# Kernel optimization log

Measured on AMD Instinct MI355X. Metric: run time of the kernel, lower is better.

The kernel has to match this reference:

```python
import jax, jax.numpy as jnp
from jax import lax
import numpy as np

B, L, D, H, SH = 4, 1024, 512, 8, 256
MLP_H = 4 * D
GAMMA, BETA = 0.1, 1.0
SIG_A, SIG_B = 1.0, 0.5
BIG = 1e9


def setup_inputs() -> dict:
    key = jax.random.key(0)
    ks = jax.random.split(key, 8)

    def lin(k, fin, fout):
        return jax.random.normal(k, (fin, fout), jnp.float32) * (1.0 / np.sqrt(fin))

    inp = {}
    inp["x"] = jax.random.normal(ks[0], (B, L, D), jnp.float32)
    inp["ln1_g"] = jnp.ones((D,), jnp.float32)
    inp["ln1_b"] = jnp.zeros((D,), jnp.float32)
    inp["ln2_g"] = jnp.ones((D,), jnp.float32)
    inp["ln2_b"] = jnp.zeros((D,), jnp.float32)
    inp["qkv_w"] = lin(ks[1], D, 3 * D)
    inp["qkv_b"] = jnp.zeros((3 * D,), jnp.float32)
    inp["proj_w"] = lin(ks[2], D, D)
    inp["proj_b"] = jnp.zeros((D,), jnp.float32)
    inp["fc1_w"] = lin(ks[3], D, MLP_H)
    inp["fc1_b"] = jnp.zeros((MLP_H,), jnp.float32)
    inp["fc2_w"] = lin(ks[4], MLP_H, D)
    inp["fc2_b"] = jnp.zeros((D,), jnp.float32)
    # 4 SigmaNets (norm1, attn, norm2, mlp) stacked on leading axis
    inp["sig_w1"] = jax.random.normal(ks[5], (4, D, SH), jnp.float32) * (1.0 / np.sqrt(D))
    inp["sig_b1"] = jnp.zeros((4, SH), jnp.float32)
    inp["sig_w2"] = jax.random.normal(ks[6], (4, SH, D), jnp.float32) * (1.0 / np.sqrt(SH))
    inp["sig_b2"] = jnp.zeros((4, D), jnp.float32)
    return inp


def layernorm(x, g, b, eps=1e-5):
    m = x.mean(-1, keepdims=True)
    v = ((x - m) ** 2).mean(-1, keepdims=True)
    return (x - m) / jnp.sqrt(v + eps) * g + b


def sigmanet(x, w1, b1, w2, b2):
    # (B,L,D) -> (B,L,1), sigma = a*sigmoid(mean(fc2(relu(fc1(x))))) + b
    h = jax.nn.relu(x @ w1 + b1)
    o = h @ w2 + b2
    m = o.mean(-1, keepdims=True)
    return SIG_A * jax.nn.sigmoid(m) + SIG_B


def attention(x, qkv_w, qkv_b, proj_w, proj_b):
    b_, l_, d_ = x.shape
    hd = d_ // H
    qkv = (x @ qkv_w + qkv_b).reshape(b_, l_, 3, H, hd)
    q, k, v = qkv[:, :, 0], qkv[:, :, 1], qkv[:, :, 2]  # (B,L,H,hd)
    scores = jnp.einsum("bqhd,bkhd->bhqk", q, k) * (hd ** -0.5)
    attn = jax.nn.softmax(scores, axis=-1)
    out = jnp.einsum("bhqk,bkhd->bqhd", attn, v).reshape(b_, l_, d_)
    return out @ proj_w + proj_b


def mlp(x, fc1_w, fc1_b, fc2_w, fc2_b):
    return jax.nn.gelu(x @ fc1_w + fc1_b, approximate=False) @ fc2_w + fc2_b


def soft_dtw(C, gamma):
    # soft-min DP over (B, N, N) cost matrix via anti-diagonal scan
    b_, n_, m_ = C.shape
    i_arr = jnp.arange(n_)

    def step(carry, k):
        d2, d1 = carry  # diagonals k-2, k-1; entry i holds R[i, (k-?)-i]
        j = k - i_arr
        valid = (j >= 0) & (j < m_)
        jc = jnp.clip(j, 0, m_ - 1)
        Cd = jnp.where(valid[None, :], C[:, i_arr, jc], BIG)
        pad = jnp.full((b_, 1), BIG, C.dtype)
        a = jnp.concatenate([pad, d2[:, :-1]], axis=1)  # R[i-1, j-1]
        a = a.at[:, 0].set(jnp.where(k == 0, 0.0, a[:, 0]))  # virtual R[-1,-1]=0
        bdiag = jnp.concatenate([pad, d1[:, :-1]], axis=1)  # R[i-1, j]
        c = d1  # R[i, j-1]
        smin = -gamma * jax.nn.logsumexp(-jnp.stack([a, bdiag, c], 0) / gamma, axis=0)
        new = jnp.where(valid[None, :], Cd + smin, BIG)
        return (d1, new), None

    init = (jnp.full((b_, n_), BIG, C.dtype), jnp.full((b_, n_), BIG, C.dtype))
    (_, last), _ = lax.scan(step, init, jnp.arange(n_ + m_ - 1))
    return last[:, n_ - 1]  # R[N-1, M-1]


def udtw(x, y, sx, sy):
    # pairwise squared distances without (B,L,L,D) intermediate
    x2 = jnp.sum(x * x, -1)  # (B,L)
    y2 = jnp.sum(y * y, -1)
    Dm = x2[:, :, None] + y2[:, None, :] - 2.0 * jnp.einsum("bnd,bmd->bnm", x, y)
    Dm = jnp.maximum(Dm, 0.0)
    Sig = sx ** 2 + jnp.swapaxes(sy, 1, 2) ** 2  # (B,L,L) sigma_i^2 + sigma_j^2
    d = soft_dtw(Dm / Sig, GAMMA)               # uncertainty-weighted distance path
    s = soft_dtw(BETA * jnp.log(Sig), GAMMA)    # sigma regularization path
    return d, s


def reference(x, ln1_g, ln1_b, ln2_g, ln2_b, qkv_w, qkv_b, proj_w, proj_b,
              fc1_w, fc1_b, fc2_w, fc2_b, sig_w1, sig_b1, sig_w2, sig_b2):
    orig = x
    attn_out = attention(layernorm(x, ln1_g, ln1_b), qkv_w, qkv_b, proj_w, proj_b)
    sigma_x = sigmanet(orig, sig_w1[0], sig_b1[0], sig_w2[0], sig_b2[0])
    sigma_attn = sigmanet(attn_out, sig_w1[1], sig_b1[1], sig_w2[1], sig_b2[1])
    d_a, s_a = udtw(orig, attn_out, sigma_x, sigma_attn)
    x = x + attn_out * sigma_attn  # merge_mode == 'mul'
    mlp_out = mlp(layernorm(x, ln2_g, ln2_b), fc1_w, fc1_b, fc2_w, fc2_b)
    sigma_x2 = sigmanet(orig, sig_w1[2], sig_b1[2], sig_w2[2], sig_b2[2])
    sigma_mlp = sigmanet(mlp_out, sig_w1[3], sig_b1[3], sig_w2[3], sig_b2[3])
    d_m, s_m = udtw(orig, mlp_out, sigma_x2, sigma_mlp)
    l_ = x.shape[1]
    aux_loss = (d_a.mean() + s_a.mean() + d_m.mean() + s_m.mean()) / (l_ * l_)
    x = x + mlp_out * sigma_mlp
    return x, aux_loss
```

## Files before the change

### kernel.cpp

```cpp
#include <hip/hip_runtime.h>
#include <math.h>

typedef unsigned short ushort;
typedef __attribute__((ext_vector_type(8))) short short8;
typedef __attribute__((ext_vector_type(4))) short short4v;
typedef __attribute__((ext_vector_type(4))) float f32x4;

#define DEVI static __device__ __forceinline__

constexpr int Bq = 4, Lq = 1024, Dq = 512, Hq = 8, SHq = 256;
constexpr int Mrows = Bq * Lq;
constexpr float BIGF = 1e9f;
constexpr int PSTR = 1048576 + 16;

DEVI float bf2f(ushort u) { union { unsigned u; float f; } v; v.u = ((unsigned)u) << 16; return v.f; }
DEVI float bf2f(short s) { return bf2f((ushort)s); }
DEVI ushort f2bf(float f) {
  union { float f; unsigned u; } v; v.f = f;
  unsigned r = v.u + 0x7fffu + ((v.u >> 16) & 1u);
  return (ushort)(r >> 16);
}
DEVI float wave_sum(float x) { for (int o = 1; o < 64; o <<= 1) x += __shfl_xor(x, o, 64); return x; }
DEVI float readin(const void* p, long i, int isf32) {
  return isf32 ? ((const float*)p)[i] : bf2f(((const ushort*)p)[i]);
}
DEVI float sigm05(float x) { return 1.f / (1.f + __expf(-x)) + 0.5f; }

DEVI void gload16(const ushort* g, ushort* l) {
  __builtin_amdgcn_global_load_lds((const __attribute__((address_space(1))) unsigned*)g,
                                   (__attribute__((address_space(3))) unsigned*)l, 16, 0, 0);
}

__global__ void detect_kern(const unsigned* __restrict__ g, int* __restrict__ flag) {
  if (threadIdx.x == 0) flag[0] = (g[0] == 0x3F800000u) ? 1 : 0;
}

struct PrepArgs {
  const void *ln1_g, *ln1_b, *ln2_g, *ln2_b, *qkv_b, *proj_b, *fc1_b, *fc2_b, *sig_b1;
  ushort* csmall;
  const void* x_raw; ushort* x_bf;
  const void *qkv_w, *proj_w, *fc1_w, *fc2_w, *sig_w1;
  ushort *wt_qkv, *wt_proj, *wt_fc1, *wt_fc2, *wt_sig1;
  const void *sig_w2;
  const void *sig_b2;
  float *w2bar, *b2bar;
  float *zbuf;
  const int* flag;
};

DEVI void do_transpose(const void* src, ushort* dst, int R, int C, int bx, int by, int bz, int f,
                       ushort (*t)[65]) {
  const int tx = threadIdx.x & 63, tg = threadIdx.x >> 6;
  const long base = (long)bz * R * C;
  const int r0 = by * 64, c0 = bx * 64;
#pragma unroll
  for (int i = 0; i < 16; ++i) {
    int y = tg * 16 + i;
    float v = readin(src, base + (long)(r0 + y) * C + c0 + tx, f);
    t[y][tx] = f2bf(v);
  }
  __syncthreads();
#pragma unroll
  for (int i = 0; i < 16; ++i) {
    int y = tg * 16 + i;
    dst[base + (long)(c0 + y) * R + r0 + tx] = t[tx][y];
  }
}

__global__ __launch_bounds__(256) void prep_kern(PrepArgs a) {
  __shared__ ushort t[64][65];
  const int bid = blockIdx.x, tid = threadIdx.x;
  const int f = *a.flag;
  if (bid < 9) {
    const int off[10] = {0, 512, 1024, 1536, 2048, 3584, 4096, 6144, 6656, 7680};
    const void* ps[9] = {a.ln1_g, a.ln1_b, a.ln2_g, a.ln2_b, a.qkv_b, a.proj_b, a.fc1_b, a.fc2_b, a.sig_b1};
    const void* s = ps[bid];
    const int n = off[bid + 1] - off[bid];
    for (int i = tid; i < n; i += 256)
      a.csmall[off[bid] + i] = f ? f2bf(((const float*)s)[i]) : ((const ushort*)s)[i];
  } else if (bid < 2057) {
    const long c0 = (long)(bid - 9) * 1024;
    for (int i = tid; i < 1024; i += 256)
      a.x_bf[c0 + i] = f ? f2bf(((const float*)a.x_raw)[c0 + i]) : ((const ushort*)a.x_raw)[c0 + i];
  } else if (bid < 2313) {
    const int wid = tid >> 6, lane = tid & 63;
    const int p = (bid - 2057) * 4 + wid;
    const int k = p & 255, s = p >> 8;
    float acc = 0.f;
#pragma unroll
    for (int i = 0; i < 8; ++i) acc += readin(a.sig_w2, ((long)s * SHq + k) * Dq + lane * 8 + i, f);
    acc = wave_sum(acc);
    if (lane == 0) a.w2bar[s * SHq + k] = acc * (1.f / Dq);
  } else if (bid < 2314) {
    const int wid = tid >> 6, lane = tid & 63;
    float acc = 0.f;
#pragma unroll
    for (int i = 0; i < 8; ++i) acc += readin(a.sig_b2, (long)wid * Dq + lane * 8 + i, f);
    acc = wave_sum(acc);
    if (lane == 0) a.b2bar[wid] = acc * (1.f / Dq);
  } else if (bid < 2506) {
    const int lb = bid - 2314;
    do_transpose(a.qkv_w, a.wt_qkv, 512, 1536, lb % 24, lb / 24, 0, f, t);
  } else if (bid < 2570) {
    const int lb = bid - 2506;
    do_transpose(a.proj_w, a.wt_proj, 512, 512, lb % 8, lb / 8, 0, f, t);
  } else if (bid < 2826) {
    const int lb = bid - 2570;
    do_transpose(a.fc1_w, a.wt_fc1, 512, 2048, lb % 32, lb / 32, 0, f, t);
  } else if (bid < 3082) {
    const int lb = bid - 2826;
    do_transpose(a.fc2_w, a.wt_fc2, 2048, 512, lb % 8, lb / 8, 0, f, t);
  } else if (bid < 3210) {
    const int lb = bid - 3082;
    const int z = lb / 32, rem = lb % 32;
    do_transpose(a.sig_w1, a.wt_sig1, 512, 256, rem % 4, rem / 4, z, f, t);
  } else {
    const int base = (bid - 3210) * 1024;
    for (int i = tid; i < 1024; i += 256) a.zbuf[base + i] = 0.f;
  }
}

__global__ __launch_bounds__(256) void ln_kern(const ushort* __restrict__ x, const ushort* __restrict__ g,
                                               const ushort* __restrict__ b, ushort* __restrict__ out,
                                               float* __restrict__ x2out) {
  const int row = blockIdx.x * 4 + (threadIdx.x >> 6);
  const int lane = threadIdx.x & 63;
  short8 v = *(const short8*)(x + (long)row * Dq + lane * 8);
  float f[8]; float s = 0.f, s2 = 0.f;
#pragma unroll
  for (int i = 0; i < 8; ++i) { f[i] = bf2f(v[i]); s += f[i]; s2 += f[i] * f[i]; }
  s = wave_sum(s); s2 = wave_sum(s2);
  if (lane == 0) x2out[row] = s2;
  float mean = s * (1.f / Dq);
  float var = s2 * (1.f / Dq) - mean * mean;
  float rstd = rsqrtf(var + 1e-5f);
  short8 gv = *(const short8*)(g + lane * 8);
  short8 bv = *(const short8*)(b + lane * 8);
  short8 o;
#pragma unroll
  for (int i = 0; i < 8; ++i) o[i] = (short)f2bf((f[i] - mean) * rstd * bf2f(gv[i]) + bf2f(bv[i]));
  *(short8*)(out + (long)row * Dq + lane * 8) = o;
}

template<int EPI>
__global__ __launch_bounds__(256) void gemm_kern(
    const ushort* __restrict__ A, int lda, long sA,
    const ushort* __restrict__ Bt, int ldb, long sB,
    const ushort* __restrict__ bias,
    void* __restrict__ Cout, int ldc, long sC, int K,
    float* __restrict__ ysq,
    const float* __restrict__ w2bar_base, float* __restrict__ sdot, int setBase, int setStep,
    const float* __restrict__ vx2, const float* __restrict__ vy2,
    const float* __restrict__ dotx, const float* __restrict__ doty,
    const float* __restrict__ b2bar, int setx, int sety) {
  __shared__ alignas(16) ushort As[128 * 32];
  __shared__ alignas(16) ushort Bs[128 * 32];
  const int tid = threadIdx.x, lane = tid & 63, wid = tid >> 6;
  const int wr = wid >> 1, wc = wid & 1;
  const int m0 = blockIdx.y * 128, n0 = blockIdx.x * 128;
  const int bz = blockIdx.z;
  const ushort* Ab = A + (long)bz * sA;
  const ushort* Bb = Bt + (long)bz * sB;
  const int lr = lane & 15, lk = (lane >> 4) * 8;
  const int srow = lane >> 2, scol = (lane & 3) * 8;
  f32x4 acc[4][4];
#pragma unroll
  for (int i = 0; i < 4; ++i)
#pragma unroll
    for (int j = 0; j < 4; ++j) acc[i][j] = f32x4{0.f, 0.f, 0.f, 0.f};

  for (int k0 = 0; k0 < K; k0 += 32) {
    __syncthreads();
    {
      const int rA0 = wid * 16, rA1 = wid * 16 + 64;
      gload16(Ab + (long)(m0 + rA0 + srow) * lda + k0 + scol, &As[rA0 * 32]);
      gload16(Ab + (long)(m0 + rA1 + srow) * lda + k0 + scol, &As[rA1 * 32]);
      gload16(Bb + (long)(n0 + rA0 + srow) * ldb + k0 + scol, &Bs[rA0 * 32]);
      gload16(Bb + (long)(n0 + rA1 + srow) * ldb + k0 + scol, &Bs[rA1 * 32]);
    }
    __syncthreads();
    short8 af[4], bg[4];
#pragma unroll
    for (int m = 0; m < 4; ++m) af[m] = *(const short8*)&As[(wr * 64 + m * 16 + lr) * 32 + lk];
#pragma unroll
    for (int n = 0; n < 4; ++n) bg[n] = *(const short8*)&Bs[(wc * 64 + n * 16 + lr) * 32 + lk];
#pragma unroll
    for (int m = 0; m < 4; ++m)
#pragma unroll
      for (int n = 0; n < 4; ++n)
        acc[m][n] = __builtin_amdgcn_mfma_f32_16x16x32_bf16(af[m], bg[n], acc[m][n], 0, 0, 0);
  }
  const int lq = (lane >> 4) * 4;
  const int set = (EPI == 1) ? (setBase + bz * setStep) : 0;
  float pd[4][4];
  if (EPI == 1 || (EPI == 0 && ysq != nullptr)) {
#pragma unroll
    for (int m = 0; m < 4; ++m)
#pragma unroll
      for (int q = 0; q < 4; ++q) pd[m][q] = 0.f;
  }
#pragma unroll
  for (int n = 0; n < 4; ++n) {
    const int col = n0 + wc * 64 + n * 16 + lr;
    float bia = 0.f, y2v = 0.f, syv = 0.f, w2v = 0.f;
    if (EPI == 0 || EPI == 2) { if (bias) bia = bf2f(bias[col]); }
    if (EPI == 1) { bia = bf2f(bias[set * 256 + col]); w2v = w2bar_base[set * SHq + col]; }
    if (EPI == 3) {
      y2v = vy2[(long)bz * Lq + col];
      float t = sigm05(doty[(long)bz * Lq + col] + b2bar[sety]);
      syv = t * t;
    }
#pragma unroll
    for (int m = 0; m < 4; ++m) {
      f32x4 v = acc[m][n];
      if (EPI == 0 || EPI == 2) {
#pragma unroll
        for (int q = 0; q < 4; ++q) {
          const int row = m0 + wr * 64 + m * 16 + lq + q;
          float c = v[q] + bia;
          if (EPI == 2) c = 0.5f * c * (1.f + erff(c * 0.70710678118654752f));
          ushort cb = f2bf(c);
          ((ushort*)Cout)[(long)bz * sC + (long)row * ldc + col] = cb;
          if (EPI == 0 && ysq != nullptr) { float cr = bf2f(cb); pd[m][q] += cr * cr; }
        }
      } else if (EPI == 1) {
#pragma unroll
        for (int q = 0; q < 4; ++q) {
          float c = fmaxf(v[q] + bia, 0.f);
          pd[m][q] += f2bf(c) == 0 ? 0.f : bf2f(f2bf(c)) * w2v;
        }
      } else {
        const int row0 = m0 + wr * 64 + m * 16 + lq;
        f32x4 o;
#pragma unroll
        for (int q = 0; q < 4; ++q) {
          float x2v = vx2[(long)bz * Lq + row0 + q];
          float t = sigm05(dotx[(long)bz * Lq + row0 + q] + b2bar[setx]);
          float dm = fmaxf(x2v + y2v - 2.f * v[q], 0.f);
          o[q] = dm / (t * t + syv);
        }
        *(f32x4*)((float*)Cout + (long)bz * sC + (long)col * 1024 + row0) = o;
      }
    }
  }
  if (EPI == 1 || (EPI == 0 && ysq != nullptr)) {
#pragma unroll
    for (int m = 0; m < 4; ++m)
#pragma unroll
      for (int q = 0; q < 4; ++q) {
#pragma unroll
        for (int o = 1; o < 16; o <<= 1) pd[m][q] += __shfl_xor(pd[m][q], o, 64);
        if (lr == 0) {
          const int row = m0 + wr * 64 + m * 16 + lq + q;
          if (EPI == 1) atomicAdd(&sdot[(long)set * Mrows + row], pd[m][q]);
          else          atomicAdd(&ysq[row], pd[m][q]);
        }
      }
  }
}

__global__ __launch_bounds__(256) void attn_kern(const ushort* __restrict__ qkv, ushort* __restrict__ octx) {
  const int qt = blockIdx.x, h = blockIdx.y, b = blockIdx.z;
  const int tid = threadIdx.x, lane = tid & 63, wid = tid >> 6;
  const int lr = lane & 15, lkg = lane >> 4;
  __shared__ alignas(16) short Ks[64 * 72];
  __shared__ alignas(16) short Vt[64 * 72];
  __shared__ alignas(16) short Ps[64 * 72];
  const long qrow0 = (long)b * Lq + qt * 64;
  short8 qf[2];
  {
    const ushort* qp = qkv + (qrow0 + wid * 16 + lr) * 1536 + h * 64;
    qf[0] = *(const short8*)(qp + lkg * 8);
    qf[1] = *(const short8*)(qp + 32 + lkg * 8);
  }
  f32x4 accO[4];
#pragma unroll
  for (int n = 0; n < 4; ++n) accO[n] = f32x4{0.f, 0.f, 0.f, 0.f};
  float mrun[4], lrun[4];
#pragma unroll
  for (int q = 0; q < 4; ++q) { mrun[q] = -1e30f; lrun[q] = 0.f; }

  for (int t = 0; t < 16; ++t) {
    __syncthreads();
#pragma unroll
    for (int i = 0; i < 2; ++i) {
      const int row = (tid >> 3) + i * 32;
      const int c8 = (tid & 7) * 8;
      const long gr = ((long)b * Lq + t * 64 + row) * 1536 + h * 64;
      short8 kv = *(const short8*)(qkv + gr + 512 + c8);
      *(short8*)&Ks[row * 72 + c8] = kv;
      short8 vv = *(const short8*)(qkv + gr + 1024 + c8);
#pragma unroll
      for (int j = 0; j < 8; ++j) Vt[(c8 + j) * 72 + row] = vv[j];
    }
    __syncthreads();
    f32x4 sf[4];
#pragma unroll
    for (int n = 0; n < 4; ++n) {
      sf[n] = f32x4{0.f, 0.f, 0.f, 0.f};
#pragma unroll
      for (int ks = 0; ks < 2; ++ks) {
        short8 bk = *(const short8*)&Ks[(n * 16 + lr) * 72 + ks * 32 + lkg * 8];
        sf[n] = __builtin_amdgcn_mfma_f32_16x16x32_bf16(qf[ks], bk, sf[n], 0, 0, 0);
      }
    }
#pragma unroll
    for (int n = 0; n < 4; ++n)
#pragma unroll
      for (int q = 0; q < 4; ++q) sf[n][q] *= 0.125f;
    float scl[4];
#pragma unroll
    for (int q = 0; q < 4; ++q) {
      float mx = fmaxf(fmaxf(sf[0][q], sf[1][q]), fmaxf(sf[2][q], sf[3][q]));
#pragma unroll
      for (int o = 1; o < 16; o <<= 1) mx = fmaxf(mx, __shfl_xor(mx, o, 64));
      float mnew = fmaxf(mrun[q], mx);
      scl[q] = __expf(mrun[q] - mnew);
      mrun[q] = mnew;
      float rs = 0.f;
#pragma unroll
      for (int n = 0; n < 4; ++n) { float pp = __expf(sf[n][q] - mnew); sf[n][q] = pp; rs += pp; }
#pragma unroll
      for (int o = 1; o < 16; o <<= 1) rs += __shfl_xor(rs, o, 64);
      lrun[q] = lrun[q] * scl[q] + rs;
    }
#pragma unroll
    for (int n = 0; n < 4; ++n)
#pragma unroll
      for (int q = 0; q < 4; ++q) accO[n][q] *= scl[q];
#pragma unroll
    for (int n = 0; n < 4; ++n)
#pragma unroll
      for (int q = 0; q < 4; ++q)
        Ps[(wid * 16 + lkg * 4 + q) * 72 + n * 16 + lr] = (short)f2bf(sf[n][q]);
    short8 pa[2];
    pa[0] = *(const short8*)&Ps[(wid * 16 + lr) * 72 + lkg * 8];
    pa[1] = *(const short8*)&Ps[(wid * 16 + lr) * 72 + 32 + lkg * 8];
#pragma unroll
    for (int n = 0; n < 4; ++n)
#pragma unroll
      for (int ks = 0; ks < 2; ++ks) {
        short8 bv = *(const short8*)&Vt[(n * 16 + lr) * 72 + ks * 32 + lkg * 8];
        accO[n] = __builtin_amdgcn_mfma_f32_16x16x32_bf16(pa[ks], bv, accO[n], 0, 0, 0);
      }
  }
#pragma unroll
  for (int n = 0; n < 4; ++n) {
    const int col = h * 64 + n * 16 + lr;
#pragma unroll
    for (int q = 0; q < 4; ++q) {
      const long row = qrow0 + wid * 16 + lkg * 4 + q;
      octx[row * 512 + col] = f2bf(accO[n][q] / fmaxf(lrun[q], 1e-30f));
    }
  }
}

__global__ __launch_bounds__(256) void fuse1_kern(const ushort* __restrict__ x, const ushort* __restrict__ attn,
                                                  const float* __restrict__ sdot1, const float* __restrict__ b2bar,
                                                  const ushort* __restrict__ g,
                                                  const ushort* __restrict__ bb, void* __restrict__ x1out,
                                                  ushort* __restrict__ xn2, const int* __restrict__ flag) {
  const int row = blockIdx.x * 4 + (threadIdx.x >> 6), lane = threadIdx.x & 63;
  const int isf32 = *flag;
  const float sg = sigm05(sdot1[row] + b2bar[1]);
  short8 xv = *(const short8*)(x + (long)row * Dq + lane * 8);
  short8 av = *(const short8*)(attn + (long)row * Dq + lane * 8);
  float f[8]; float s = 0.f, s2 = 0.f;
#pragma unroll
  for (int i = 0; i < 8; ++i) {
    f[i] = bf2f(xv[i]) + bf2f(av[i]) * sg;
    s += f[i]; s2 += f[i] * f[i];
  }
  if (isf32) {
    float* o32 = (float*)x1out + (long)row * Dq + lane * 8;
    *(f32x4*)o32 = f32x4{f[0], f[1], f[2], f[3]};
    *(f32x4*)(o32 + 4) = f32x4{f[4], f[5], f[6], f[7]};
  } else {
    short8 xo;
#pragma unroll
    for (int i = 0; i < 8; ++i) xo[i] = (short)f2bf(f[i]);
    *(short8*)((ushort*)x1out + (long)row * Dq + lane * 8) = xo;
  }
  s = wave_sum(s); s2 = wave_sum(s2);
  float mean = s * (1.f / Dq);
  float var = s2 * (1.f / Dq) - mean * mean;
  float rstd = rsqrtf(var + 1e-5f);
  short8 gv = *(const short8*)(g + lane * 8);
  short8 bv = *(const short8*)(bb + lane * 8);
  short8 o;
#pragma unroll
  for (int i = 0; i < 8; ++i) o[i] = (short)f2bf((f[i] - mean) * rstd * bf2f(gv[i]) + bf2f(bv[i]));
  *(short8*)(xn2 + (long)row * Dq + lane * 8) = o;
}

__global__ __launch_bounds__(256) void fuse2_kern(const ushort* __restrict__ mlp,
                                                  const float* __restrict__ sdot3, const float* __restrict__ b2bar,
                                                  void* __restrict__ out, const int* __restrict__ flag) {
  const int row = blockIdx.x * 4 + (threadIdx.x >> 6), lane = threadIdx.x & 63;
  const int isf32 = *flag;
  const float sg = sigm05(sdot3[row] + b2bar[3]);
  short8 mv = *(const short8*)(mlp + (long)row * Dq + lane * 8);
  if (isf32) {
    float* o32 = (float*)out + (long)row * Dq + lane * 8;
    f32x4 a = *(const f32x4*)o32;
    f32x4 b = *(const f32x4*)(o32 + 4);
#pragma unroll
    for (int i = 0; i < 4; ++i) a[i] += bf2f(mv[i]) * sg;
#pragma unroll
    for (int i = 0; i < 4; ++i) b[i] += bf2f(mv[4 + i]) * sg;
    *(f32x4*)o32 = a;
    *(f32x4*)(o32 + 4) = b;
  } else {
    ushort* o16 = (ushort*)out + (long)row * Dq + lane * 8;
    short8 xv = *(const short8*)o16;
    short8 o;
#pragma unroll
    for (int i = 0; i < 8; ++i) o[i] = (short)f2bf(bf2f(xv[i]) + bf2f(mv[i]) * sg);
    *(short8*)o16 = o;
  }
}

__global__ __launch_bounds__(128, 1) void dtw_kern(const float* __restrict__ Cta, const float* __restrict__ Ctm,
                                                   const float* __restrict__ sdot, const float* __restrict__ b2bar,
                                                   float* __restrict__ res) {
  const int sid = blockIdx.x >> 2, b = blockIdx.x & 3;
  const int tid = threadIdx.x, lane = tid & 63, wid = tid >> 6;
  const bool isS = (sid & 1);
  __shared__ alignas(16) float smemf[18432];
  constexpr float LN2 = 0.69314718055994531f;

  float cur[16];
#pragma unroll
  for (int r = 0; r < 16; ++r) cur[r] = BIGF;
  float A = BIGF;
  float B = BIGF;
  float D = (lane == 0) ? 0.f : BIGF;

  if (!isS) {
    const float* Ct = ((sid == 0) ? Cta : Ctm) + (long)b * PSTR;

#define PRODUCE2(S0)                                                           \
    {                                                                          \
      f32x4 L[4][8];                                                           \
      _Pragma("unroll")                                                        \
      for (int j = 0; j < 4; ++j) {                                            \
        const int ss = (S0) + j;                                               \
        int cA = 2 * ss - 2 * lane;                                            \
        int cB = cA + 1;                                                       \
        cA = cA < 0 ? 0 : (cA > 1023 ? 1023 : cA);                             \
        cB = cB < 0 ? 0 : (cB > 1023 ? 1023 : cB);                             \
        const float* gA = Ct + (long)cA * 1024 + lane * 16;                    \
        const float* gB = Ct + (long)cB * 1024 + lane * 16;                    \
        _Pragma("unroll")                                                      \
        for (int q = 0; q < 4; ++q) { L[j][q] = *(const f32x4*)(gA + q * 4);   \
                                      L[j][4 + q] = *(const f32x4*)(gB + q * 4); } \
      }                                                                        \
      __builtin_amdgcn_sched_barrier(0);                                       \
      _Pragma("unroll")                                                        \
      for (int j = 0; j < 4; ++j) {                                            \
        float* lp = &smemf[(((S0) + j) & 7) * 2304 + lane * 36];               \
        _Pragma("unroll")                                                      \
        for (int q = 0; q < 4; ++q) { *(f32x4*)(lp + q * 4) = L[j][q];         \
                                      *(f32x4*)(lp + 16 + q * 4) = L[j][4 + q]; } \
      }                                                                        \
    }

#define LOADR(RA, RB, S)                                                       \
    {                                                                          \
      const float* lp = &smemf[((S) & 7) * 2304 + lane * 36];                  \
      _Pragma("unroll")                                                        \
      for (int q = 0; q < 4; ++q) { RA[q] = *(const f32x4*)(lp + q * 4);       \
                                    RB[q] = *(const f32x4*)(lp + 16 + q * 4); } \
    }

#define DCHAIN2(S, RA, RB, CHK)                                                \
    {                                                                          \
      const int c1 = 2 * (S) - 2 * lane;                                       \
      const bool v1 = (unsigned)c1 < 1024u;                                    \
      const bool v2 = (unsigned)(c1 + 1) < 1024u;                              \
      float above = A, diag = D;                                               \
      _Pragma("unroll")                                                        \
      for (int i = 0; i < 16; ++i) {                                           \
        float tmp = cur[i];                                                    \
        float v = RA[i >> 2][i & 3] + fminf(fminf(above, tmp), diag);          \
        cur[i] = (CHK) ? (v1 ? v : tmp) : v;                                   \
        diag = tmp; above = v;                                                 \
      }                                                                        \
      float bot1 = cur[15];                                                    \
      above = B; diag = A;                                                     \
      _Pragma("unroll")                                                        \
      for (int i = 0; i < 16; ++i) {                                           \
        float tmp = cur[i];                                                    \
        float v = RB[i >> 2][i & 3] + fminf(fminf(above, tmp), diag);          \
        cur[i] = (CHK) ? (v2 ? v : tmp) : v;                                   \
        diag = tmp; above = v;                                                 \
      }                                                                        \
      float bot2 = cur[15];                                                    \
      D = B;                                                                   \
      float sA = __shfl_up(bot1, 1, 64);                                       \
      float sB = __shfl_up(bot2, 1, 64);                                       \
      A = (lane == 0) ? BIGF : sA;                                             \
      B = (lane == 0) ? BIGF : sB;                                             \
    }

#define DPHASE4(S0, CHK)                                                       \
    {                                                                          \
      f32x4 pa[4], pb[4], qa[4], qb[4];                                        \
      LOADR(pa, pb, (S0) + 0)                                                  \
      LOADR(qa, qb, (S0) + 1)                                                  \
      DCHAIN2((S0) + 0, pa, pb, CHK)                                           \
      LOADR(pa, pb, (S0) + 2)                                                  \
      DCHAIN2((S0) + 1, qa, qb, CHK)                                           \
      LOADR(qa, qb, (S0) + 3)                                                  \
      DCHAIN2((S0) + 2, pa, pb, CHK)                                           \
      DCHAIN2((S0) + 3, qa, qb, CHK)                                           \
    }

    if (wid == 1) PRODUCE2(0)
    __syncthreads();
#pragma clang loop unroll(disable)
    for (int p = 0; p < 16; ++p) {
      if (wid == 1) { PRODUCE2(4 * p + 4) } else { DPHASE4(4 * p, 1) }
      __syncthreads();
    }
#pragma clang loop unroll(disable)
    for (int p = 16; p < 128; ++p) {
      if (wid == 1) { PRODUCE2(4 * p + 4) } else { DPHASE4(4 * p, 0) }
      __syncthreads();
    }
#pragma clang loop unroll(disable)
    for (int p = 128; p < 144; ++p) {
      if (wid == 1) { if (p < 143) PRODUCE2(4 * p + 4) } else { DPHASE4(4 * p, 1) }
      __syncthreads();
    }
#undef PRODUCE2
#undef LOADR
#undef DCHAIN2
#undef DPHASE4
    if (wid == 0 && lane == 63) res[blockIdx.x] = cur[15];
  } else {
    const int sxset = (sid == 1) ? 0 : 2;
    const float bx2 = b2bar[sxset], by2 = b2bar[sxset + 1];
    const float* dx = sdot + (long)sxset * Mrows + b * Lq;
    const float* dy = sdot + (long)(sxset + 1) * Mrows + b * Lq;
    for (int i = tid; i < Lq; i += 128) { float v = sigm05(dy[i] + by2); smemf[i] = v * v; }
    __syncthreads();
    if (wid == 1) return;
    float sx2[16];
#pragma unroll
    for (int r = 0; r < 16; ++r) { float t = sigm05(dx[16 * lane + r] + bx2); sx2[r] = t * t; }
    int ia = -2 * lane; ia = ia < 0 ? 0 : ia;
    int ib = 1 - 2 * lane; ib = ib < 0 ? 0 : ib;
    float syA = smemf[ia], syB = smemf[ib];

#define SSTEP2(S, CHK)                                                         \
    {                                                                          \
      int na = 2 * ((S) + 1) - 2 * lane; na = na < 0 ? 0 : (na > 1023 ? 1023 : na); \
      int nb = na + 1; nb = nb > 1023 ? 1023 : nb;                             \
      float syA_n = smemf[na], syB_n = smemf[nb];                              \
      const int c1 = 2 * (S) - 2 * lane;                                       \
      const bool v1 = (unsigned)c1 < 1024u;                                    \
      const bool v2 = (unsigned)(c1 + 1) < 1024u;                              \
      float above = A, diag = D;                                               \
      _Pragma("unroll")                                                        \
      for (int i = 0; i < 16; ++i) {                                           \
        float tmp = cur[i];                                                    \
        float cv = LN2 * __builtin_amdgcn_logf(sx2[i] + syA);                  \
        float v = cv + fminf(fminf(above, tmp), diag);                         \
        cur[i] = (CHK) ? (v1 ? v : tmp) : v;                                   \
        diag = tmp; above = v;                                                 \
      }                                                                        \
      float bot1 = cur[15];                                                    \
      above = B; diag = A;                                                     \
      _Pragma("unroll")                                                        \
      for (int i = 0; i < 16; ++i) {                                           \
        float tmp = cur[i];                                                    \
        float cv = LN2 * __builtin_amdgcn_logf(sx2[i] + syB);                  \
        float v = cv + fminf(fminf(above, tmp), diag);                         \
        cur[i] = (CHK) ? (v2 ? v : tmp) : v;                                   \
        diag = tmp; above = v;                                                 \
      }                                                                        \
      float bot2 = cur[15];                                                    \
      D = B; syA = syA_n; syB = syB_n;                                         \
      float sA = __shfl_up(bot1, 1, 64);                                       \
      float sB = __shfl_up(bot2, 1, 64);                                       \
      A = (lane == 0) ? BIGF : sA;                                             \
      B = (lane == 0) ? BIGF : sB;                                             \
    }

#pragma clang loop unroll(disable)
    for (int s = 0; s < 63; ++s) SSTEP2(s, 1)
#pragma clang loop unroll(disable)
    for (int s = 63; s < 512; ++s) SSTEP2(s, 0)
#pragma clang loop unroll(disable)
    for (int s = 512; s < 576; ++s) SSTEP2(s, 1)
#undef SSTEP2
    if (lane == 63) res[blockIdx.x] = cur[15];
  }
}

__global__ void aux_kern(const float* __restrict__ res, void* __restrict__ out,
                         const int* __restrict__ flag) {
  if (threadIdx.x == 0) {
    float s = 0.f;
    for (int i = 0; i < 16; ++i) s += res[i];
    float v = s * (0.25f / (1024.f * 1024.f));
    if (*flag) ((float*)out)[(size_t)Mrows * 512] = v;
    else       ((ushort*)out)[(size_t)Mrows * 512] = f2bf(v);
  }
}

extern "C" void kernel_launch(void* const* d_in, const int* in_sizes, int n_in,
                              void* d_out, int out_size, void* d_ws, size_t ws_size,
                              hipStream_t stream) {
  const void* x_raw   = d_in[0];
  const void* ln1_g   = d_in[1];
  const void* ln1_b   = d_in[2];
  const void* ln2_g   = d_in[3];
  const void* ln2_b   = d_in[4];
  const void* qkv_w   = d_in[5];
  const void* qkv_b   = d_in[6];
  const void* proj_w  = d_in[7];
  const void* proj_b  = d_in[8];
  const void* fc1_w   = d_in[9];
  const void* fc1_b   = d_in[10];
  const void* fc2_w   = d_in[11];
  const void* fc2_b   = d_in[12];
  const void* sig_w1  = d_in[13];
  const void* sig_b1  = d_in[14];
  const void* sig_w2  = d_in[15];
  const void* sig_b2  = d_in[16];

  char* p = (char*)d_ws;
  auto alloc = [&](size_t n) { char* r = p; p += (n + 255) & ~(size_t)255; return r; };
  const size_t REGION = (size_t)4 * PSTR * 4;
  int*    flag    = (int*)alloc(256);
  ushort* csmall  = (ushort*)alloc(7680 * 2);
  ushort* x_bf    = (ushort*)alloc((size_t)Mrows * 512 * 2);
  ushort* wt_qkv  = (ushort*)alloc((size_t)1536 * 512 * 2);
  ushort* wt_proj = (ushort*)alloc((size_t)512 * 512 * 2);
  ushort* wt_fc1  = (ushort*)alloc((size_t)2048 * 512 * 2);
  ushort* wt_fc2  = (ushort*)alloc((size_t)512 * 2048 * 2);
  ushort* wt_sig1 = (ushort*)alloc((size_t)4 * 256 * 512 * 2);
  float*  w2bar   = (float*)alloc(4 * 256 * 4);
  float*  b2bar   = (float*)alloc(4 * 4);
  ushort* xnorm   = (ushort*)alloc((size_t)Mrows * 512 * 2);
  char* region1 = alloc(REGION);
  ushort* qkvb     = (ushort*)region1;
  ushort* attn_ctx = (ushort*)(region1 + (size_t)Mrows * 1536 * 2);
  float*  Cta      = (float*)region1;
  ushort* abuf   = (ushort*)alloc((size_t)Mrows * 512 * 2);
  float*  sdot   = (float*)alloc((size_t)4 * Mrows * 4);
  float*  y2a    = (float*)alloc(Mrows * 4);
  float*  y2m    = (float*)alloc(Mrows * 4);
  float*  x2n    = (float*)alloc(Mrows * 4);
  char* region2 = alloc(REGION);
  ushort* h1  = (ushort*)region2;
  float*  Ctm = (float*)region2;
  float*  dres = (float*)alloc(64 * 4);

  const ushort* c_ln1g = csmall + 0;
  const ushort* c_ln1b = csmall + 512;
  const ushort* c_ln2g = csmall + 1024;
  const ushort* c_ln2b = csmall + 1536;
  const ushort* c_qkvb = csmall + 2048;
  const ushort* c_projb = csmall + 3584;
  const ushort* c_fc1b = csmall + 4096;
  const ushort* c_fc2b = csmall + 6144;
  const ushort* c_sigb1 = csmall + 6656;

  detect_kern<<<1, 64, 0, stream>>>((const unsigned*)ln1_g, flag);
  PrepArgs pa;
  pa.ln1_g = ln1_g; pa.ln1_b = ln1_b; pa.ln2_g = ln2_g; pa.ln2_b = ln2_b;
  pa.qkv_b = qkv_b; pa.proj_b = proj_b; pa.fc1_b = fc1_b; pa.fc2_b = fc2_b; pa.sig_b1 = sig_b1;
  pa.csmall = csmall; pa.x_raw = x_raw; pa.x_bf = x_bf;
  pa.qkv_w = qkv_w; pa.proj_w = proj_w; pa.fc1_w = fc1_w; pa.fc2_w = fc2_w; pa.sig_w1 = sig_w1;
  pa.wt_qkv = wt_qkv; pa.wt_proj = wt_proj; pa.wt_fc1 = wt_fc1; pa.wt_fc2 = wt_fc2; pa.wt_sig1 = wt_sig1;
  pa.sig_w2 = sig_w2; pa.sig_b2 = sig_b2; pa.w2bar = w2bar; pa.b2bar = b2bar;
  pa.zbuf = sdot; pa.flag = flag;
  prep_kern<<<3234, 256, 0, stream>>>(pa);

  ln_kern<<<Mrows / 4, 256, 0, stream>>>(x_bf, c_ln1g, c_ln1b, xnorm, x2n);
  gemm_kern<0><<<dim3(12, 32, 1), 256, 0, stream>>>(xnorm, 512, 0, wt_qkv, 512, 0, c_qkvb,
      qkvb, 1536, 0, 512, nullptr, nullptr, nullptr, 0, 0, nullptr, nullptr, nullptr, nullptr, nullptr, 0, 0);
  attn_kern<<<dim3(16, 8, 4), 256, 0, stream>>>(qkvb, attn_ctx);
  gemm_kern<0><<<dim3(4, 32, 1), 256, 0, stream>>>(attn_ctx, 512, 0, wt_proj, 512, 0, c_projb,
      abuf, 512, 0, 512, y2a, nullptr, nullptr, 0, 0, nullptr, nullptr, nullptr, nullptr, nullptr, 0, 0);
  gemm_kern<1><<<dim3(2, 32, 2), 256, 0, stream>>>(x_bf, 512, 0, wt_sig1, 512, (long)2 * 256 * 512, c_sigb1,
      nullptr, 0, 0, 512, nullptr, w2bar, sdot, 0, 2, nullptr, nullptr, nullptr, nullptr, nullptr, 0, 0);
  gemm_kern<1><<<dim3(2, 32, 1), 256, 0, stream>>>(abuf, 512, 0, wt_sig1 + 1 * 256 * 512, 512, 0, c_sigb1,
      nullptr, 0, 0, 512, nullptr, w2bar, sdot, 1, 0, nullptr, nullptr, nullptr, nullptr, nullptr, 0, 0);
  gemm_kern<3><<<dim3(8, 8, 4), 256, 0, stream>>>(x_bf, 512, (long)1024 * 512, abuf, 512, (long)1024 * 512, nullptr,
      Cta, 1024, (long)PSTR, 512, nullptr, nullptr, nullptr, 0, 0, x2n, y2a, sdot, sdot + Mrows, b2bar, 0, 1);
  fuse1_kern<<<Mrows / 4, 256, 0, stream>>>(x_bf, abuf, sdot + Mrows, b2bar, c_ln2g, c_ln2b, d_out, xnorm, flag);
  gemm_kern<2><<<dim3(16, 32, 1), 256, 0, stream>>>(xnorm, 512, 0, wt_fc1, 512, 0, c_fc1b,
      h1, 2048, 0, 512, nullptr, nullptr, nullptr, 0, 0, nullptr, nullptr, nullptr, nullptr, nullptr, 0, 0);
  gemm_kern<0><<<dim3(4, 32, 1), 256, 0, stream>>>(h1, 2048, 0, wt_fc2, 2048, 0, c_fc2b,
      abuf, 512, 0, 2048, y2m, nullptr, nullptr, 0, 0, nullptr, nullptr, nullptr, nullptr, nullptr, 0, 0);
  gemm_kern<1><<<dim3(2, 32, 1), 256, 0, stream>>>(abuf, 512, 0, wt_sig1 + 3 * 256 * 512, 512, 0, c_sigb1,
      nullptr, 0, 0, 512, nullptr, w2bar, sdot, 3, 0, nullptr, nullptr, nullptr, nullptr, nullptr, 0, 0);
  gemm_kern<3><<<dim3(8, 8, 4), 256, 0, stream>>>(x_bf, 512, (long)1024 * 512, abuf, 512, (long)1024 * 512, nullptr,
      Ctm, 1024, (long)PSTR, 512, nullptr, nullptr, nullptr, 0, 0, x2n, y2m, sdot + 2 * Mrows, sdot + 3 * Mrows, b2bar, 2, 3);
  fuse2_kern<<<Mrows / 4, 256, 0, stream>>>(abuf, sdot + 3 * Mrows, b2bar, d_out, flag);
  dtw_kern<<<16, 128, 0, stream>>>(Cta, Ctm, sdot, b2bar, dres);
  aux_kern<<<1, 64, 0, stream>>>(dres, d_out, flag);
}
```

Before: 497.5 us.

## Process four DTW columns per wavefront step and fold aux reduction into DTW kernel

The DTW wavefront now advances four columns per lane per step instead of two. That halves the number of lane-shift steps and block barriers in the serial chain (319 steps instead of 576 half-steps). The producer warp stages four column slices into a 4-deep LDS ring, and LDS use shrinks slightly. The separate aux_kern launch is removed: the last finishing DTW block, detected with an atomic counter reset in detect_kern, sums the 16 results and writes the aux loss. The wider diagonal skew adds more wasted masked work at the start and end, and holds more registers per step.

```diff
diff --git a/kernel.cpp b/kernel.cpp
--- a/kernel.cpp
+++ b/kernel.cpp
@@ -31,8 +31,12 @@
                                    (__attribute__((address_space(3))) unsigned*)l, 16, 0, 0);
 }
 
-__global__ void detect_kern(const unsigned* __restrict__ g, int* __restrict__ flag) {
-  if (threadIdx.x == 0) flag[0] = (g[0] == 0x3F800000u) ? 1 : 0;
+__global__ void detect_kern(const unsigned* __restrict__ g, int* __restrict__ flag,
+                            float* res, unsigned* cnt) {
+  const int t = threadIdx.x;
+  if (t == 0) flag[0] = (g[0] == 0x3F800000u) ? 1 : 0;
+  if (t < 16) res[t] = 0.f;
+  if (t == 16) *cnt = 0u;
 }
 
 struct PrepArgs {
@@ -422,122 +426,100 @@
 
 __global__ __launch_bounds__(128, 1) void dtw_kern(const float* __restrict__ Cta, const float* __restrict__ Ctm,
                                                    const float* __restrict__ sdot, const float* __restrict__ b2bar,
-                                                   float* __restrict__ res) {
+                                                   float* res, unsigned* cnt,
+                                                   void* __restrict__ out, const int* __restrict__ flag) {
   const int sid = blockIdx.x >> 2, b = blockIdx.x & 3;
   const int tid = threadIdx.x, lane = tid & 63, wid = tid >> 6;
   const bool isS = (sid & 1);
-  __shared__ alignas(16) float smemf[18432];
+  __shared__ alignas(16) float smemf[17408];
   constexpr float LN2 = 0.69314718055994531f;
+  constexpr int NSTEP = 319;
 
   float cur[16];
 #pragma unroll
   for (int r = 0; r < 16; ++r) cur[r] = BIGF;
-  float A = BIGF;
-  float B = BIGF;
+  float A0 = BIGF, A1 = BIGF, A2 = BIGF, A3 = BIGF;
   float D = (lane == 0) ? 0.f : BIGF;
 
   if (!isS) {
     const float* Ct = ((sid == 0) ? Cta : Ctm) + (long)b * PSTR;
 
-#define PRODUCE2(S0)                                                           \
+#define PRODUCE4(S)                                                            \
     {                                                                          \
-      f32x4 L[4][8];                                                           \
+      f32x4 L[16];                                                             \
       _Pragma("unroll")                                                        \
       for (int j = 0; j < 4; ++j) {                                            \
-        const int ss = (S0) + j;                                               \
-        int cA = 2 * ss - 2 * lane;                                            \
-        int cB = cA + 1;                                                       \
-        cA = cA < 0 ? 0 : (cA > 1023 ? 1023 : cA);                             \
-        cB = cB < 0 ? 0 : (cB > 1023 ? 1023 : cB);                             \
-        const float* gA = Ct + (long)cA * 1024 + lane * 16;                    \
-        const float* gB = Ct + (long)cB * 1024 + lane * 16;                    \
+        int c = 4 * (S) + j - 4 * lane;                                        \
+        c = c < 0 ? 0 : (c > 1023 ? 1023 : c);                                 \
+        const float* gp = Ct + (long)c * 1024 + lane * 16;                     \
         _Pragma("unroll")                                                      \
-        for (int q = 0; q < 4; ++q) { L[j][q] = *(const f32x4*)(gA + q * 4);   \
-                                      L[j][4 + q] = *(const f32x4*)(gB + q * 4); } \
+        for (int q = 0; q < 4; ++q) L[j * 4 + q] = *(const f32x4*)(gp + q * 4);\
       }                                                                        \
       __builtin_amdgcn_sched_barrier(0);                                       \
+      float* lp = &smemf[((S) & 3) * 4352 + lane * 68];                        \
       _Pragma("unroll")                                                        \
-      for (int j = 0; j < 4; ++j) {                                            \
-        float* lp = &smemf[(((S0) + j) & 7) * 2304 + lane * 36];               \
+      for (int j = 0; j < 4; ++j)                                              \
         _Pragma("unroll")                                                      \
-        for (int q = 0; q < 4; ++q) { *(f32x4*)(lp + q * 4) = L[j][q];         \
-                                      *(f32x4*)(lp + 16 + q * 4) = L[j][4 + q]; } \
-      }                                                                        \
-    }
-
-#define LOADR(RA, RB, S)                                                       \
+        for (int q = 0; q < 4; ++q) *(f32x4*)(lp + j * 16 + q * 4) = L[j * 4 + q]; \
+    }
+
+#define DCOL(RV, AV, DV, VC, CHK)                                              \
     {                                                                          \
-      const float* lp = &smemf[((S) & 7) * 2304 + lane * 36];                  \
-      _Pragma("unroll")                                                        \
-      for (int q = 0; q < 4; ++q) { RA[q] = *(const f32x4*)(lp + q * 4);       \
-                                    RB[q] = *(const f32x4*)(lp + 16 + q * 4); } \
-    }
-
-#define DCHAIN2(S, RA, RB, CHK)                                                \
-    {                                                                          \
-      const int c1 = 2 * (S) - 2 * lane;                                       \
-      const bool v1 = (unsigned)c1 < 1024u;                                    \
-      const bool v2 = (unsigned)(c1 + 1) < 1024u;                              \
-      float above = A, diag = D;                                               \
+      float above = AV, diag = DV;                                             \
       _Pragma("unroll")                                                        \
       for (int i = 0; i < 16; ++i) {                                           \
         float tmp = cur[i];                                                    \
-        float v = RA[i >> 2][i & 3] + fminf(fminf(above, tmp), diag);          \
-        cur[i] = (CHK) ? (v1 ? v : tmp) : v;                                   \
+        float v = RV[i >> 2][i & 3] + fminf(fminf(above, tmp), diag);          \
+        cur[i] = (CHK) ? ((VC) ? v : tmp) : v;                                 \
         diag = tmp; above = v;                                                 \
       }                                                                        \
-      float bot1 = cur[15];                                                    \
-      above = B; diag = A;                                                     \
+    }
+
+#define DSTEP4(S, CHK)                                                         \
+    {                                                                          \
+      const float* lp = &smemf[((S) & 3) * 4352 + lane * 68];                  \
+      f32x4 R0[4], R1[4], R2[4], R3[4];                                        \
       _Pragma("unroll")                                                        \
-      for (int i = 0; i < 16; ++i) {                                           \
-        float tmp = cur[i];                                                    \
-        float v = RB[i >> 2][i & 3] + fminf(fminf(above, tmp), diag);          \
-        cur[i] = (CHK) ? (v2 ? v : tmp) : v;                                   \
-        diag = tmp; above = v;                                                 \
-      }                                                                        \
-      float bot2 = cur[15];                                                    \
-      D = B;                                                                   \
-      float sA = __shfl_up(bot1, 1, 64);                                       \
-      float sB = __shfl_up(bot2, 1, 64);                                       \
-      A = (lane == 0) ? BIGF : sA;                                             \
-      B = (lane == 0) ? BIGF : sB;                                             \
-    }
-
-#define DPHASE4(S0, CHK)                                                       \
-    {                                                                          \
-      f32x4 pa[4], pb[4], qa[4], qb[4];                                        \
-      LOADR(pa, pb, (S0) + 0)                                                  \
-      LOADR(qa, qb, (S0) + 1)                                                  \
-      DCHAIN2((S0) + 0, pa, pb, CHK)                                           \
-      LOADR(pa, pb, (S0) + 2)                                                  \
-      DCHAIN2((S0) + 1, qa, qb, CHK)                                           \
-      LOADR(qa, qb, (S0) + 3)                                                  \
-      DCHAIN2((S0) + 2, pa, pb, CHK)                                           \
-      DCHAIN2((S0) + 3, qa, qb, CHK)                                           \
-    }
-
-    if (wid == 1) PRODUCE2(0)
+      for (int q = 0; q < 4; ++q) { R0[q] = *(const f32x4*)(lp + q * 4);       \
+                                    R1[q] = *(const f32x4*)(lp + 16 + q * 4);  \
+                                    R2[q] = *(const f32x4*)(lp + 32 + q * 4);  \
+                                    R3[q] = *(const f32x4*)(lp + 48 + q * 4); }\
+      const int c0 = 4 * (S) - 4 * lane;                                       \
+      const bool v0 = (unsigned)c0 < 1024u;                                    \
+      const bool v1 = (unsigned)(c0 + 1) < 1024u;                              \
+      const bool v2 = (unsigned)(c0 + 2) < 1024u;                              \
+      const bool v3 = (unsigned)(c0 + 3) < 1024u;                              \
+      DCOL(R0, A0, D, v0, CHK)  float b0 = cur[15];                            \
+      DCOL(R1, A1, A0, v1, CHK) float b1 = cur[15];                            \
+      DCOL(R2, A2, A1, v2, CHK) float b2 = cur[15];                            \
+      DCOL(R3, A3, A2, v3, CHK) float b3 = cur[15];                            \
+      D = A3;                                                                  \
+      float s0 = __shfl_up(b0, 1, 64), s1 = __shfl_up(b1, 1, 64);              \
+      float s2 = __shfl_up(b2, 1, 64), s3 = __shfl_up(b3, 1, 64);              \
+      A0 = (lane == 0) ? BIGF : s0; A1 = (lane == 0) ? BIGF : s1;              \
+      A2 = (lane == 0) ? BIGF : s2; A3 = (lane == 0) ? BIGF : s3;              \
+    }
+
+    if (wid == 1) { PRODUCE4(0) PRODUCE4(1) PRODUCE4(2) }
     __syncthreads();
 #pragma clang loop unroll(disable)
-    for (int p = 0; p < 16; ++p) {
-      if (wid == 1) { PRODUCE2(4 * p + 4) } else { DPHASE4(4 * p, 1) }
+    for (int p = 0; p < 63; ++p) {
+      if (wid == 1) { PRODUCE4(p + 3) } else { DSTEP4(p, 1) }
       __syncthreads();
     }
 #pragma clang loop unroll(disable)
-    for (int p = 16; p < 128; ++p) {
-      if (wid == 1) { PRODUCE2(4 * p + 4) } else { DPHASE4(4 * p, 0) }
+    for (int p = 63; p < 256; ++p) {
+      if (wid == 1) { PRODUCE4(p + 3) } else { DSTEP4(p, 0) }
       __syncthreads();
     }
 #pragma clang loop unroll(disable)
-    for (int p = 128; p < 144; ++p) {
-      if (wid == 1) { if (p < 143) PRODUCE2(4 * p + 4) } else { DPHASE4(4 * p, 1) }
+    for (int p = 256; p < NSTEP; ++p) {
+      if (wid == 1) { if (p + 3 < NSTEP) PRODUCE4(p + 3) } else { DSTEP4(p, 1) }
       __syncthreads();
     }
-#undef PRODUCE2
-#undef LOADR
-#undef DCHAIN2
-#undef DPHASE4
-    if (wid == 0 && lane == 63) res[blockIdx.x] = cur[15];
+#undef PRODUCE4
+#undef DCOL
+#undef DSTEP4
   } else {
     const int sxset = (sid == 1) ? 0 : 2;
     const float bx2 = b2bar[sxset], by2 = b2bar[sxset + 1];
@@ -545,68 +527,67 @@
     const float* dy = sdot + (long)(sxset + 1) * Mrows + b * Lq;
     for (int i = tid; i < Lq; i += 128) { float v = sigm05(dy[i] + by2); smemf[i] = v * v; }
     __syncthreads();
-    if (wid == 1) return;
-    float sx2[16];
-#pragma unroll
-    for (int r = 0; r < 16; ++r) { float t = sigm05(dx[16 * lane + r] + bx2); sx2[r] = t * t; }
-    int ia = -2 * lane; ia = ia < 0 ? 0 : ia;
-    int ib = 1 - 2 * lane; ib = ib < 0 ? 0 : ib;
-    float syA = smemf[ia], syB = smemf[ib];
-
-#define SSTEP2(S, CHK)                                                         \
-    {                                                                          \
-      int na = 2 * ((S) + 1) - 2 * lane; na = na < 0 ? 0 : (na > 1023 ? 1023 : na); \
-      int nb = na + 1; nb = nb > 1023 ? 1023 : nb;                             \
-      float syA_n = smemf[na], syB_n = smemf[nb];                              \
-      const int c1 = 2 * (S) - 2 * lane;                                       \
-      const bool v1 = (unsigned)c1 < 1024u;                                    \
-      const bool v2 = (unsigned)(c1 + 1) < 1024u;                              \
-      float above = A, diag = D;                                               \
-      _Pragma("unroll")                                                        \
-      for (int i = 0; i < 16; ++i) {                                           \
-        float tmp = cur[i];                                                    \
-        float cv = LN2 * __builtin_amdgcn_logf(sx2[i] + syA);                  \
-        float v = cv + fminf(fminf(above, tmp), diag);                         \
-        cur[i] = (CHK) ? (v1 ? v : tmp) : v;                                   \
-        diag = tmp; above = v;                                                 \
-      }                                                                        \
-      float bot1 = cur[15];                                                    \
-      above = B; diag = A;                                                     \
-      _Pragma("unroll")                                                        \
-      for (int i = 0; i < 16; ++i) {                                           \
-        float tmp = cur[i];                                                    \
-        float cv = LN2 * __builtin_amdgcn_logf(sx2[i] + syB);                  \
-        float v = cv + fminf(fminf(above, tmp), diag);                         \
-        cur[i] = (CHK) ? (v2 ? v : tmp) : v;                                   \
-        diag = tmp; above = v;                                                 \
-      }                                                                        \
-      float bot2 = cur[15];                                                    \
-      D = B; syA = syA_n; syB = syB_n;                                         \
-      float sA = __shfl_up(bot1, 1, 64);                                       \
-      float sB = __shfl_up(bot2, 1, 64);                                       \
-      A = (lane == 0) ? BIGF : sA;                                             \
-      B = (lane == 0) ? BIGF : sB;                                             \
-    }
+    if (wid == 0) {
+      float sx2[16];
+#pragma unroll
+      for (int r = 0; r < 16; ++r) { float t = sigm05(dx[16 * lane + r] + bx2); sx2[r] = t * t; }
+
+#define SCOL(SYV, AV, DV, VC, CHK)                                             \
+      {                                                                        \
+        float above = AV, diag = DV;                                           \
+        _Pragma("unroll")                                                      \
+        for (int i = 0; i < 16; ++i) {                                         \
+          float tmp = cur[i];                                                  \
+          float cv = LN2 * __builtin_amdgcn_logf(sx2[i] + SYV);                \
+          float v = cv + fminf(fminf(above, tmp), diag);                       \
+          cur[i] = (CHK) ? ((VC) ? v : tmp) : v;                               \
+          diag = tmp; above = v;                                               \
+        }                                                                      \
+      }
+
+#define SSTEP4(S, CHK)                                                         \
+      {                                                                        \
+        const int c0 = 4 * (S) - 4 * lane;                                     \
+        int cc = c0 < 0 ? 0 : (c0 > 1020 ? 1020 : c0);                         \
+        float y0 = smemf[cc], y1 = smemf[cc + 1], y2 = smemf[cc + 2], y3 = smemf[cc + 3]; \
+        const bool v0 = (unsigned)c0 < 1024u;                                  \
+        const bool v1 = (unsigned)(c0 + 1) < 1024u;                            \
+        const bool v2 = (unsigned)(c0 + 2) < 1024u;                            \
+        const bool v3 = (unsigned)(c0 + 3) < 1024u;                            \
+        SCOL(y0, A0, D, v0, CHK)  float b0 = cur[15];                          \
+        SCOL(y1, A1, A0, v1, CHK) float b1 = cur[15];                          \
+        SCOL(y2, A2, A1, v2, CHK) float b2 = cur[15];                          \
+        SCOL(y3, A3, A2, v3, CHK) float b3 = cur[15];                          \
+        D = A3;                                                                \
+        float s0 = __shfl_up(b0, 1, 64), s1 = __shfl_up(b1, 1, 64);            \
+        float s2 = __shfl_up(b2, 1, 64), s3 = __shfl_up(b3, 1, 64);            \
+        A0 = (lane == 0) ? BIGF : s0; A1 = (lane == 0) ? BIGF : s1;            \
+        A2 = (lane == 0) ? BIGF : s2; A3 = (lane == 0) ? BIGF : s3;            \
+      }
 
 #pragma clang loop unroll(disable)
-    for (int s = 0; s < 63; ++s) SSTEP2(s, 1)
+      for (int s = 0; s < 63; ++s) SSTEP4(s, 1)
 #pragma clang loop unroll(disable)
-    for (int s = 63; s < 512; ++s) SSTEP2(s, 0)
+      for (int s = 63; s < 256; ++s) SSTEP4(s, 0)
 #pragma clang loop unroll(disable)
-    for (int s = 512; s < 576; ++s) SSTEP2(s, 1)
-#undef SSTEP2
-    if (lane == 63) res[blockIdx.x] = cur[15];
-  }
-}
-
-__global__ void aux_kern(const float* __restrict__ res, void* __restrict__ out,
-                         const int* __restrict__ flag) {
-  if (threadIdx.x == 0) {
-    float s = 0.f;
-    for (int i = 0; i < 16; ++i) s += res[i];
-    float v = s * (0.25f / (1024.f * 1024.f));
-    if (*flag) ((float*)out)[(size_t)Mrows * 512] = v;
-    else       ((ushort*)out)[(size_t)Mrows * 512] = f2bf(v);
+      for (int s = 256; s < NSTEP; ++s) SSTEP4(s, 1)
+#undef SCOL
+#undef SSTEP4
+    }
+  }
+  if (wid == 0 && lane == 63) {
+    res[blockIdx.x] = cur[15];
+    __threadfence();
+    unsigned old = atomicAdd(cnt, 1u);
+    if (old == 15u) {
+      __threadfence();
+      volatile float* vres = res;
+      float ssum = 0.f;
+      for (int i = 0; i < 16; ++i) ssum += vres[i];
+      float v = ssum * (0.25f / (1024.f * 1024.f));
+      if (*flag) ((float*)out)[(size_t)Mrows * 512] = v;
+      else       ((ushort*)out)[(size_t)Mrows * 512] = f2bf(v);
+    }
   }
 }
 
@@ -654,10 +635,11 @@
   float*  y2a    = (float*)alloc(Mrows * 4);
   float*  y2m    = (float*)alloc(Mrows * 4);
   float*  x2n    = (float*)alloc(Mrows * 4);
+  float*  dres   = (float*)alloc(64 * 4);
+  unsigned* dcnt = (unsigned*)(dres + 32);
   char* region2 = alloc(REGION);
   ushort* h1  = (ushort*)region2;
   float*  Ctm = (float*)region2;
-  float*  dres = (float*)alloc(64 * 4);
 
   const ushort* c_ln1g = csmall + 0;
   const ushort* c_ln1b = csmall + 512;
@@ -669,7 +651,7 @@
   const ushort* c_fc2b = csmall + 6144;
   const ushort* c_sigb1 = csmall + 6656;
 
-  detect_kern<<<1, 64, 0, stream>>>((const unsigned*)ln1_g, flag);
+  detect_kern<<<1, 64, 0, stream>>>((const unsigned*)ln1_g, flag, dres, dcnt);
   PrepArgs pa;
   pa.ln1_g = ln1_g; pa.ln1_b = ln1_b; pa.ln2_g = ln2_g; pa.ln2_b = ln2_b;
   pa.qkv_b = qkv_b; pa.proj_b = proj_b; pa.fc1_b = fc1_b; pa.fc2_b = fc2_b; pa.sig_b1 = sig_b1;
@@ -702,6 +684,5 @@
   gemm_kern<3><<<dim3(8, 8, 4), 256, 0, stream>>>(x_bf, 512, (long)1024 * 512, abuf, 512, (long)1024 * 512, nullptr,
       Ctm, 1024, (long)PSTR, 512, nullptr, nullptr, nullptr, 0, 0, x2n, y2m, sdot + 2 * Mrows, sdot + 3 * Mrows, b2bar, 2, 3);
   fuse2_kern<<<Mrows / 4, 256, 0, stream>>>(abuf, sdot + 3 * Mrows, b2bar, d_out, flag);
-  dtw_kern<<<16, 128, 0, stream>>>(Cta, Ctm, sdot, b2bar, dres);
-  aux_kern<<<1, 64, 0, stream>>>(dres, d_out, flag);
-}
+  dtw_kern<<<16, 128, 0, stream>>>(Cta, Ctm, sdot, b2bar, dres, dcnt, d_out, flag);
+}
```

Result: slower. 516.8 us (+3.9%).
